# Kernel tuning notes

Hardware: AMD Instinct MI355X
Metric: run time of the kernel (lower is better)

The kernel has to match this reference:

```python
import jax, jax.numpy as jnp
import numpy as np
import math

# SLAYER SRM-alpha neuron / simulation constants (from netParams yaml)
THETA = 10.0     # spike threshold
TAU_SR = 10.0    # PSP (srm) kernel time constant
TAU_REF = 1.0    # refractory kernel time constant
SCALE_REF = 2.0  # refractory kernel scale
TS = 1.0         # simulation timestep
POOL_GAIN = 1.1 * THETA  # SLAYER pool: sum over window scaled by 1.1*theta

# alpha kernel eps(t) = (t/tau) * exp(1 - t/tau); at lag L*Ts this equals
# (e*Ts/tau) * L * d**L with d = exp(-Ts/tau). Convolution with it is computed
# by a fused two-state linear recurrence (lax.scan over time), matching the
# fused-scan structure of the original SLAYER CUDA kernels.

def psp(x):
    """Leaky temporal integration: x [..., T] -> psp [..., T]."""
    d = math.exp(-TS / TAU_SR)
    B = math.e * TS / TAU_SR
    xt = jnp.moveaxis(x, -1, 0)  # [T, ...]
    z = jnp.zeros_like(xt[0])
    def step(carry, xn):
        p, q = carry
        q = d * (q + p)          # q_n = sum_{m<n} x[m] (n-m) d^(n-m)
        p = d * p + xn           # p_n = sum_{m<=n} x[m] d^(n-m)
        return (p, q), B * q
    _, out = jax.lax.scan(step, (z, z), xt)
    return jnp.moveaxis(out, 0, -1)


def spike(u):
    """Threshold spike generation with refractory feedback (SRM).
    u [..., T] membrane drive -> binary spikes [..., T].
    Refractory kernel: -scaleRef*theta * (t/tauRef) * exp(1 - t/tauRef).
    """
    d = math.exp(-TS / TAU_REF)
    A = -SCALE_REF * THETA * math.e * TS / TAU_REF
    ut = jnp.moveaxis(u, -1, 0)
    z = jnp.zeros_like(ut[0])
    def surr(v):
        # hard threshold forward, sigmoid surrogate gradient (straight-through)
        hard = (v >= THETA).astype(v.dtype)
        soft = jax.nn.sigmoid((v - THETA) * (4.0 / THETA))
        return soft + jax.lax.stop_gradient(hard - soft)
    def step(carry, un):
        p, q = carry
        q = d * (q + p)
        s = surr(un + A * q)  # membrane = drive + refractory response
        p = d * p + s
        return (p, q), s
    _, out = jax.lax.scan(step, (z, z), ut)
    return jnp.moveaxis(out, 0, -1)


def conv_t(x, w, pad):
    """Per-timestep 2D conv on [N,C,H,W,T]; kernel w [O,I,kh,kw]."""
    return jax.lax.conv_general_dilated(
        x, w[..., None], window_strides=(1, 1, 1),
        padding=[(pad, pad), (pad, pad), (0, 0)],
        dimension_numbers=("NCHWT", "OIHWT", "NCHWT"))


def pool2(x):
    """SLAYER 2x2 sum-pool scaled by 1.1*theta, per timestep."""
    N, C, H, W, T = x.shape
    return x.reshape(N, C, H // 2, 2, W // 2, 2, T).sum(axis=(3, 5)) * POOL_GAIN


def dense_t(x, w):
    """Dense over (C,H,W) per timestep: x [N,C,H,W,T], w [O,C,H,W] -> [N,O,T]."""
    return jnp.einsum("nchwt,ochw->not", x, w)


def setup_inputs() -> dict:
    key = jax.random.key(0)
    k0, k1, k2, k3, k4 = jax.random.split(key, 5)
    spikeInput = (jax.random.uniform(k0, (8, 1, 30, 30, 300)) < 0.05).astype(jnp.float32)
    conv1_w = jax.random.normal(k1, (16, 1, 5, 5), jnp.float32) * 1.0
    conv2_w = jax.random.normal(k2, (32, 16, 3, 3), jnp.float32) * 0.5
    conv3_w = jax.random.normal(k3, (64, 32, 3, 3), jnp.float32) * 0.5
    fc1_w = jax.random.normal(k4, (10, 64, 7, 7), jnp.float32) * 0.5
    return {"spikeInput": spikeInput, "conv1_w": conv1_w, "conv2_w": conv2_w,
            "conv3_w": conv3_w, "fc1_w": fc1_w}


def reference(spikeInput, conv1_w, conv2_w, conv3_w, fc1_w):
    s1 = spike(conv_t(psp(spikeInput), conv1_w, pad=1))  # [8,16,28,28,300]
    s2 = spike(pool2(psp(s1)))                            # [8,16,14,14,300]
    s3 = spike(conv_t(psp(s2), conv2_w, pad=1))           # [8,32,14,14,300]
    s4 = spike(pool2(psp(s3)))                            # [8,32,7,7,300]
    s5 = spike(conv_t(psp(s4), conv3_w, pad=1))           # [8,64,7,7,300]
    out = spike(dense_t(psp(s5), fc1_w))                  # [8,10,300]
    return out
```

## Files before the change

kernel.cpp:

```cpp
#include <hip/hip_runtime.h>
#include <hip/hip_bf16.h>
#include <cstdint>

#define TT 300
#define NB 8

static constexpr float D_SR  = 0.90483741803595957f;
static constexpr float B_SR  = 0.27182818284590454f;
static constexpr float D_RF  = 0.36787944117144233f;
static constexpr float A_RF  = -54.365636569180902f;
static constexpr float THETA_F = 10.0f;
static constexpr float PGAIN = 11.0f;

__global__ void k_wtr(const float* __restrict__ w1, const float* __restrict__ w2,
                      const float* __restrict__ w3, float* __restrict__ t1,
                      float* __restrict__ t2, float* __restrict__ t3) {
    int g = blockIdx.x * blockDim.x + threadIdx.x;
    if (g < 400) {
        int oc = g / 25, s = g % 25;
        t1[s * 16 + oc] = w1[g];
    } else if (g < 400 + 4608) {
        int h = g - 400, oc = h / 144, s = h % 144;
        t2[s * 32 + oc] = w2[h];
    } else if (g < 400 + 4608 + 18432) {
        int h = g - 5008, oc = h / 288, s = h % 288;
        t3[s * 64 + oc] = w3[h];
    }
}

__global__ void k_psp_tr(const float* __restrict__ in, float* __restrict__ out, int NS) {
    int i = blockIdx.x * blockDim.x + threadIdx.x;
    if (i >= NS) return;
    const float4* x4 = (const float4*)(in + (size_t)i * TT);
    constexpr int G4 = 5;
    constexpr int NG = TT / (4 * G4);
    float4 A[G4], B[G4];
    #pragma unroll
    for (int u = 0; u < G4; ++u) A[u] = x4[u];
    float p = 0.f, q = 0.f;
    for (int g = 0; g < NG; ++g) {
        if (g + 1 < NG) {
            #pragma unroll
            for (int u = 0; u < G4; ++u) B[u] = x4[(g + 1) * G4 + u];
        }
        int t0 = g * G4 * 4;
        #pragma unroll
        for (int u = 0; u < G4; ++u) {
            float xs[4] = {A[u].x, A[u].y, A[u].z, A[u].w};
            #pragma unroll
            for (int e = 0; e < 4; ++e) {
                q = D_SR * (q + p);
                p = D_SR * p + xs[e];
                out[(size_t)(t0 + u * 4 + e) * NS + i] = B_SR * q;
            }
        }
        #pragma unroll
        for (int u = 0; u < G4; ++u) A[u] = B[u];
    }
}

template<int CI, int CO, int KS, int HI, int WI, int HO, int WO, int OCW, int J>
__global__ __launch_bounds__(256) void k_conv(const float* __restrict__ in,
                                              const float* __restrict__ wT,
                                              float* __restrict__ out) {
    constexpr int PW = WI + 2, PH = HI + 2, PST = PH * PW;
    __shared__ float lds[CI * PST];
    const int tid = threadIdx.x;
    const int tn  = blockIdx.x;
    const float* img = in + (size_t)tn * (CI * HI * WI);
    for (int idx = tid; idx < CI * PST; idx += 256) lds[idx] = 0.f;
    __syncthreads();
    for (int idx = tid; idx < CI * HI * WI; idx += 256) {
        int ic = idx / (HI * WI), rem = idx % (HI * WI);
        int r = rem / WI, c = rem % WI;
        lds[ic * PST + (r + 1) * PW + (c + 1)] = img[idx];
    }
    __syncthreads();

    const int wave = __builtin_amdgcn_readfirstlane(tid >> 6);
    const int lane = tid & 63;
    const int l = lane < 49 ? lane : 48;
    const int oc0 = (CO == OCW) ? 0 : wave * OCW;

    int pbase[J];
    #pragma unroll
    for (int j = 0; j < J; ++j) {
        int g = (CO == OCW) ? (wave * J + j) : j;
        int px = g * 49 + l;
        pbase[j] = (px / WO) * PW + (px % WO);
    }
    float acc[J * OCW];
    #pragma unroll
    for (int a = 0; a < J * OCW; ++a) acc[a] = 0.f;

    for (int ic = 0; ic < CI; ++ic) {
        #pragma unroll
        for (int kh = 0; kh < KS; ++kh) {
            #pragma unroll
            for (int kw = 0; kw < KS; ++kw) {
                const int step = (ic * KS + kh) * KS + kw;
                const float4* wv = reinterpret_cast<const float4*>(wT + step * CO + oc0);
                float4 wr[OCW / 4];
                #pragma unroll
                for (int r4 = 0; r4 < OCW / 4; ++r4) wr[r4] = wv[r4];
                const float* lw = (const float*)wr;
                #pragma unroll
                for (int j = 0; j < J; ++j) {
                    float iv = lds[ic * PST + pbase[j] + kh * PW + kw];
                    #pragma unroll
                    for (int o = 0; o < OCW; ++o) acc[j * OCW + o] += iv * lw[o];
                }
            }
        }
    }
    if (lane < 49) {
        #pragma unroll
        for (int j = 0; j < J; ++j) {
            int g = (CO == OCW) ? (wave * J + j) : j;
            int px = g * 49 + lane;
            #pragma unroll
            for (int o = 0; o < OCW; ++o)
                out[((size_t)tn * CO + oc0 + o) * (HO * WO) + px] = acc[j * OCW + o];
        }
    }
}

template<int C, int HI, int WI>
__global__ void k_fuse_pool(const float* __restrict__ U, float* __restrict__ X) {
    constexpr int HO = HI / 2, WO = WI / 2;
    constexpr int M   = NB * C * HO * WO;
    constexpr int NSI = NB * C * HI * WI;
    int i = blockIdx.x * blockDim.x + threadIdx.x;
    if (i >= M) return;
    int j = i % WO, r = (i / WO) % HO, nc = i / (WO * HO);
    size_t base = (size_t)(nc * HI + 2 * r) * WI + 2 * j;
    const float2* R0 = (const float2*)(U + base);
    const float2* R1 = (const float2*)(U + base + WI);
    constexpr int G = 10, NG = TT / G;
    float2 A0[G], A1[G], B0[G], B1[G];
    #pragma unroll
    for (int u = 0; u < G; ++u) {
        A0[u] = R0[(size_t)u * (NSI / 2)];
        A1[u] = R1[(size_t)u * (NSI / 2)];
    }
    float p00=0,q00=0,p01=0,q01=0,p10=0,q10=0,p11=0,q11=0;
    float P=0,Q=0, sp=0,sq=0, P2=0,Q2=0;
    for (int g = 0; g < NG; ++g) {
        if (g + 1 < NG) {
            #pragma unroll
            for (int u = 0; u < G; ++u) {
                B0[u] = R0[(size_t)((g + 1) * G + u) * (NSI / 2)];
                B1[u] = R1[(size_t)((g + 1) * G + u) * (NSI / 2)];
            }
        }
        #pragma unroll
        for (int u = 0; u < G; ++u) {
            int t = g * G + u;
            float s0, s1, s2, s3;
            q00 = D_RF*(q00+p00); { float v = A0[u].x + A_RF*q00; s0 = (v>=THETA_F)?1.f:0.f; } p00 = D_RF*p00+s0;
            q01 = D_RF*(q01+p01); { float v = A0[u].y + A_RF*q01; s1 = (v>=THETA_F)?1.f:0.f; } p01 = D_RF*p01+s1;
            q10 = D_RF*(q10+p10); { float v = A1[u].x + A_RF*q10; s2 = (v>=THETA_F)?1.f:0.f; } p10 = D_RF*p10+s2;
            q11 = D_RF*(q11+p11); { float v = A1[u].y + A_RF*q11; s3 = (v>=THETA_F)?1.f:0.f; } p11 = D_RF*p11+s3;
            float x = (s0 + s1 + s2 + s3) * PGAIN;
            Q = D_SR*(Q+P); P = D_SR*P + x; float drive = B_SR*Q;
            sq = D_RF*(sq+sp); float v2 = drive + A_RF*sq; float sv = (v2>=THETA_F)?1.f:0.f; sp = D_RF*sp+sv;
            Q2 = D_SR*(Q2+P2); P2 = D_SR*P2 + sv;
            X[(size_t)t * M + i] = B_SR * Q2;
        }
        #pragma unroll
        for (int u = 0; u < G; ++u) { A0[u] = B0[u]; A1[u] = B1[u]; }
    }
}

__global__ void k_spike_psp(const float* __restrict__ U, float* __restrict__ X, int NS) {
    int i = blockIdx.x * blockDim.x + threadIdx.x;
    if (i >= NS) return;
    constexpr int G = 20, NG = TT / G;
    float A[G], B[G];
    #pragma unroll
    for (int u = 0; u < G; ++u) A[u] = U[(size_t)u * NS + i];
    float p = 0, q = 0, P = 0, Q = 0;
    for (int g = 0; g < NG; ++g) {
        if (g + 1 < NG) {
            #pragma unroll
            for (int u = 0; u < G; ++u) B[u] = U[(size_t)((g + 1) * G + u) * NS + i];
        }
        #pragma unroll
        for (int u = 0; u < G; ++u) {
            int t = g * G + u;
            q = D_RF * (q + p);
            float v = A[u] + A_RF * q;
            float s = (v >= THETA_F) ? 1.f : 0.f;
            p = D_RF * p + s;
            Q = D_SR * (Q + P); P = D_SR * P + s;
            X[(size_t)t * NS + i] = B_SR * Q;
        }
        #pragma unroll
        for (int u = 0; u < G; ++u) A[u] = B[u];
    }
}

__global__ void k_dense(const float* __restrict__ X, const float* __restrict__ wf,
                        float* __restrict__ G_) {
    int tn = blockIdx.x;
    int lane = threadIdx.x;
    const float* xb = X + (size_t)tn * 3136;
    float acc[10];
    #pragma unroll
    for (int o = 0; o < 10; ++o) acc[o] = 0.f;
    for (int it = 0; it < 49; ++it) {
        int k = it * 64 + lane;
        float xv = xb[k];
        #pragma unroll
        for (int o = 0; o < 10; ++o) acc[o] += xv * wf[o * 3136 + k];
    }
    #pragma unroll
    for (int off = 32; off > 0; off >>= 1) {
        #pragma unroll
        for (int o = 0; o < 10; ++o) acc[o] += __shfl_down(acc[o], off);
    }
    if (lane == 0) {
        #pragma unroll
        for (int o = 0; o < 10; ++o) G_[tn * 10 + o] = acc[o];
    }
}

__global__ void k_spike_out(const float* __restrict__ G_, float* __restrict__ out) {
    int i = threadIdx.x;
    if (i >= 80) return;
    constexpr int G = 20, NG = TT / G;
    float A[G], B[G];
    #pragma unroll
    for (int u = 0; u < G; ++u) A[u] = G_[u * 80 + i];
    float p = 0, q = 0;
    for (int g = 0; g < NG; ++g) {
        if (g + 1 < NG) {
            #pragma unroll
            for (int u = 0; u < G; ++u) B[u] = G_[((g + 1) * G + u) * 80 + i];
        }
        #pragma unroll
        for (int u = 0; u < G; ++u) {
            int t = g * G + u;
            q = D_RF * (q + p);
            float v = A[u] + A_RF * q;
            float s = (v >= THETA_F) ? 1.f : 0.f;
            p = D_RF * p + s;
            out[(size_t)i * TT + t] = s;
        }
        #pragma unroll
        for (int u = 0; u < G; ++u) A[u] = B[u];
    }
}

static inline int cdiv(int a, int b) { return (a + b - 1) / b; }

extern "C" void kernel_launch(void* const* d_in, const int* in_sizes, int n_in,
                              void* d_out, int out_size, void* d_ws, size_t ws_size,
                              hipStream_t stream) {
    const float* x  = (const float*)d_in[0];
    const float* w1 = (const float*)d_in[1];
    const float* w2 = (const float*)d_in[2];
    const float* w3 = (const float*)d_in[3];
    const float* wf = (const float*)d_in[4];
    float* out = (float*)d_out;
    float* ws  = (float*)d_ws;

    float* A   = ws;
    float* U1  = ws + 2160000;
    float* X2  = ws + 32265600;
    float* Gg  = ws + 39792000;
    float* wT1 = ws + 39816000;
    float* wT2 = ws + 39816400;
    float* wT3 = ws + 39821008;
    float* U2  = U1;
    float* X4  = U1 + 16000000;
    float* U3  = X2;
    float* X5  = U1;

    const int B = 256;
    k_wtr<<<cdiv(23440, B), B, 0, stream>>>(w1, w2, w3, wT1, wT2, wT3);
    k_psp_tr<<<cdiv(7200, B), B, 0, stream>>>(x, A, 7200);
    k_conv<1, 16, 5, 30, 30, 28, 28, 16, 4><<<2400, B, 0, stream>>>(A, wT1, U1);
    k_fuse_pool<16, 28, 28><<<cdiv(25088, B), B, 0, stream>>>(U1, X2);
    k_conv<16, 32, 3, 14, 14, 14, 14, 32, 1><<<2400, B, 0, stream>>>(X2, wT2, U2);
    k_fuse_pool<32, 14, 14><<<cdiv(12544, B), B, 0, stream>>>(U2, X4);
    k_conv<32, 64, 3, 7, 7, 7, 7, 16, 1><<<2400, B, 0, stream>>>(X4, wT3, U3);
    k_spike_psp<<<cdiv(25088, B), B, 0, stream>>>(U3, X5, 25088);
    k_dense<<<2400, 64, 0, stream>>>(X5, wf, Gg);
    k_spike_out<<<1, 128, 0, stream>>>(Gg, out);
}
```

Measured before the change: 385.9 us.

## Split pool-fuse scan across 4 lanes, use scalar weight loads, merge prep kernels

The fused spike-pool-psp kernel now gives each of the four input pixels of a 2x2 window its own thread. The pooled sum is formed with two xor shuffles, which gives four times more threads for a kernel that had little parallelism. The conv kernels read weights through a constant address-space pointer so the compiler can use scalar loads, and the loop is reordered to load input values first. The weight-transpose and input-psp kernels are merged into one launch. The cost is that the downstream scan is computed redundantly in all four lanes, and the pool kernel now uses scalar strided loads instead of float2 loads.

```diff
diff --git a/kernel.cpp b/kernel.cpp
--- a/kernel.cpp
+++ b/kernel.cpp
@@ -12,50 +12,53 @@
 static constexpr float THETA_F = 10.0f;
 static constexpr float PGAIN = 11.0f;
 
-__global__ void k_wtr(const float* __restrict__ w1, const float* __restrict__ w2,
+typedef const float __attribute__((address_space(4)))* cfp;
+
+__global__ void k_pre(const float* __restrict__ x, float* __restrict__ A,
+                      const float* __restrict__ w1, const float* __restrict__ w2,
                       const float* __restrict__ w3, float* __restrict__ t1,
                       float* __restrict__ t2, float* __restrict__ t3) {
-    int g = blockIdx.x * blockDim.x + threadIdx.x;
-    if (g < 400) {
-        int oc = g / 25, s = g % 25;
-        t1[s * 16 + oc] = w1[g];
-    } else if (g < 400 + 4608) {
-        int h = g - 400, oc = h / 144, s = h % 144;
-        t2[s * 32 + oc] = w2[h];
-    } else if (g < 400 + 4608 + 18432) {
-        int h = g - 5008, oc = h / 288, s = h % 288;
-        t3[s * 64 + oc] = w3[h];
-    }
-}
-
-__global__ void k_psp_tr(const float* __restrict__ in, float* __restrict__ out, int NS) {
-    int i = blockIdx.x * blockDim.x + threadIdx.x;
-    if (i >= NS) return;
-    const float4* x4 = (const float4*)(in + (size_t)i * TT);
-    constexpr int G4 = 5;
-    constexpr int NG = TT / (4 * G4);
-    float4 A[G4], B[G4];
-    #pragma unroll
-    for (int u = 0; u < G4; ++u) A[u] = x4[u];
-    float p = 0.f, q = 0.f;
-    for (int g = 0; g < NG; ++g) {
-        if (g + 1 < NG) {
-            #pragma unroll
-            for (int u = 0; u < G4; ++u) B[u] = x4[(g + 1) * G4 + u];
-        }
-        int t0 = g * G4 * 4;
-        #pragma unroll
-        for (int u = 0; u < G4; ++u) {
-            float xs[4] = {A[u].x, A[u].y, A[u].z, A[u].w};
-            #pragma unroll
-            for (int e = 0; e < 4; ++e) {
-                q = D_SR * (q + p);
-                p = D_SR * p + xs[e];
-                out[(size_t)(t0 + u * 4 + e) * NS + i] = B_SR * q;
+    if (blockIdx.x < 29) {
+        const int NS = 7200;
+        int i = blockIdx.x * 256 + threadIdx.x;
+        if (i >= NS) return;
+        const float4* x4 = (const float4*)(x + (size_t)i * TT);
+        constexpr int G4 = 5, NG = TT / (4 * G4);
+        float4 Aa[G4], Bb[G4];
+        #pragma unroll
+        for (int u = 0; u < G4; ++u) Aa[u] = x4[u];
+        float p = 0.f, q = 0.f;
+        for (int g = 0; g < NG; ++g) {
+            if (g + 1 < NG) {
+                #pragma unroll
+                for (int u = 0; u < G4; ++u) Bb[u] = x4[(g + 1) * G4 + u];
             }
-        }
-        #pragma unroll
-        for (int u = 0; u < G4; ++u) A[u] = B[u];
+            int t0 = g * G4 * 4;
+            #pragma unroll
+            for (int u = 0; u < G4; ++u) {
+                float xs[4] = {Aa[u].x, Aa[u].y, Aa[u].z, Aa[u].w};
+                #pragma unroll
+                for (int e = 0; e < 4; ++e) {
+                    q = D_SR * (q + p);
+                    p = D_SR * p + xs[e];
+                    A[(size_t)(t0 + u * 4 + e) * NS + i] = B_SR * q;
+                }
+            }
+            #pragma unroll
+            for (int u = 0; u < G4; ++u) Aa[u] = Bb[u];
+        }
+    } else {
+        int g = (blockIdx.x - 29) * 256 + threadIdx.x;
+        if (g < 400) {
+            int oc = g / 25, s = g % 25;
+            t1[s * 16 + oc] = w1[g];
+        } else if (g < 400 + 4608) {
+            int h = g - 400, oc = h / 144, s = h % 144;
+            t2[s * 32 + oc] = w2[h];
+        } else if (g < 400 + 4608 + 18432) {
+            int h = g - 5008, oc = h / 288, s = h % 288;
+            t3[s * 64 + oc] = w3[h];
+        }
     }
 }
 
@@ -67,6 +70,7 @@
     __shared__ float lds[CI * PST];
     const int tid = threadIdx.x;
     const int tn  = blockIdx.x;
+    cfp wc = (cfp)(uintptr_t)wT;
     const float* img = in + (size_t)tn * (CI * HI * WI);
     for (int idx = tid; idx < CI * PST; idx += 256) lds[idx] = 0.f;
     __syncthreads();
@@ -99,16 +103,15 @@
             #pragma unroll
             for (int kw = 0; kw < KS; ++kw) {
                 const int step = (ic * KS + kh) * KS + kw;
-                const float4* wv = reinterpret_cast<const float4*>(wT + step * CO + oc0);
-                float4 wr[OCW / 4];
-                #pragma unroll
-                for (int r4 = 0; r4 < OCW / 4; ++r4) wr[r4] = wv[r4];
-                const float* lw = (const float*)wr;
-                #pragma unroll
-                for (int j = 0; j < J; ++j) {
-                    float iv = lds[ic * PST + pbase[j] + kh * PW + kw];
+                float iv[J];
+                #pragma unroll
+                for (int j = 0; j < J; ++j)
+                    iv[j] = lds[ic * PST + pbase[j] + kh * PW + kw];
+                #pragma unroll
+                for (int o = 0; o < OCW; ++o) {
+                    float wv = wc[(size_t)step * CO + oc0 + o];
                     #pragma unroll
-                    for (int o = 0; o < OCW; ++o) acc[j * OCW + o] += iv * lw[o];
+                    for (int j = 0; j < J; ++j) acc[j * OCW + o] += iv[j] * wv;
                 }
             }
         }
@@ -130,45 +133,42 @@
     constexpr int HO = HI / 2, WO = WI / 2;
     constexpr int M   = NB * C * HO * WO;
     constexpr int NSI = NB * C * HI * WI;
-    int i = blockIdx.x * blockDim.x + threadIdx.x;
+    int gth = blockIdx.x * blockDim.x + threadIdx.x;
+    int i = gth >> 2, sub = gth & 3;
     if (i >= M) return;
     int j = i % WO, r = (i / WO) % HO, nc = i / (WO * HO);
-    size_t base = (size_t)(nc * HI + 2 * r) * WI + 2 * j;
-    const float2* R0 = (const float2*)(U + base);
-    const float2* R1 = (const float2*)(U + base + WI);
+    const float* col = U + (size_t)(nc * HI + 2 * r + (sub >> 1)) * WI + 2 * j + (sub & 1);
     constexpr int G = 10, NG = TT / G;
-    float2 A0[G], A1[G], B0[G], B1[G];
-    #pragma unroll
-    for (int u = 0; u < G; ++u) {
-        A0[u] = R0[(size_t)u * (NSI / 2)];
-        A1[u] = R1[(size_t)u * (NSI / 2)];
-    }
-    float p00=0,q00=0,p01=0,q01=0,p10=0,q10=0,p11=0,q11=0;
-    float P=0,Q=0, sp=0,sq=0, P2=0,Q2=0;
+    float Aa[G], Bb[G];
+    #pragma unroll
+    for (int u = 0; u < G; ++u) Aa[u] = col[(size_t)u * NSI];
+    float p = 0, q = 0;
+    float P = 0, Q = 0, sp = 0, sq = 0, P2 = 0, Q2 = 0;
     for (int g = 0; g < NG; ++g) {
         if (g + 1 < NG) {
             #pragma unroll
-            for (int u = 0; u < G; ++u) {
-                B0[u] = R0[(size_t)((g + 1) * G + u) * (NSI / 2)];
-                B1[u] = R1[(size_t)((g + 1) * G + u) * (NSI / 2)];
-            }
+            for (int u = 0; u < G; ++u) Bb[u] = col[(size_t)((g + 1) * G + u) * NSI];
         }
         #pragma unroll
         for (int u = 0; u < G; ++u) {
             int t = g * G + u;
-            float s0, s1, s2, s3;
-            q00 = D_RF*(q00+p00); { float v = A0[u].x + A_RF*q00; s0 = (v>=THETA_F)?1.f:0.f; } p00 = D_RF*p00+s0;
-            q01 = D_RF*(q01+p01); { float v = A0[u].y + A_RF*q01; s1 = (v>=THETA_F)?1.f:0.f; } p01 = D_RF*p01+s1;
-            q10 = D_RF*(q10+p10); { float v = A1[u].x + A_RF*q10; s2 = (v>=THETA_F)?1.f:0.f; } p10 = D_RF*p10+s2;
-            q11 = D_RF*(q11+p11); { float v = A1[u].y + A_RF*q11; s3 = (v>=THETA_F)?1.f:0.f; } p11 = D_RF*p11+s3;
-            float x = (s0 + s1 + s2 + s3) * PGAIN;
-            Q = D_SR*(Q+P); P = D_SR*P + x; float drive = B_SR*Q;
-            sq = D_RF*(sq+sp); float v2 = drive + A_RF*sq; float sv = (v2>=THETA_F)?1.f:0.f; sp = D_RF*sp+sv;
-            Q2 = D_SR*(Q2+P2); P2 = D_SR*P2 + sv;
-            X[(size_t)t * M + i] = B_SR * Q2;
-        }
-        #pragma unroll
-        for (int u = 0; u < G; ++u) { A0[u] = B0[u]; A1[u] = B1[u]; }
+            q = D_RF * (q + p);
+            float v = Aa[u] + A_RF * q;
+            float s = (v >= THETA_F) ? 1.f : 0.f;
+            p = D_RF * p + s;
+            float ss = s + __shfl_xor(s, 1);
+            ss = ss + __shfl_xor(ss, 2);
+            float xv = ss * PGAIN;
+            Q = D_SR * (Q + P); P = D_SR * P + xv; float drive = B_SR * Q;
+            sq = D_RF * (sq + sp);
+            float v2 = drive + A_RF * sq;
+            float sv = (v2 >= THETA_F) ? 1.f : 0.f;
+            sp = D_RF * sp + sv;
+            Q2 = D_SR * (Q2 + P2); P2 = D_SR * P2 + sv;
+            if (sub == 0) X[(size_t)t * M + i] = B_SR * Q2;
+        }
+        #pragma unroll
+        for (int u = 0; u < G; ++u) Aa[u] = Bb[u];
     }
 }
 
@@ -176,27 +176,27 @@
     int i = blockIdx.x * blockDim.x + threadIdx.x;
     if (i >= NS) return;
     constexpr int G = 20, NG = TT / G;
-    float A[G], B[G];
-    #pragma unroll
-    for (int u = 0; u < G; ++u) A[u] = U[(size_t)u * NS + i];
+    float Aa[G], Bb[G];
+    #pragma unroll
+    for (int u = 0; u < G; ++u) Aa[u] = U[(size_t)u * NS + i];
     float p = 0, q = 0, P = 0, Q = 0;
     for (int g = 0; g < NG; ++g) {
         if (g + 1 < NG) {
             #pragma unroll
-            for (int u = 0; u < G; ++u) B[u] = U[(size_t)((g + 1) * G + u) * NS + i];
+            for (int u = 0; u < G; ++u) Bb[u] = U[(size_t)((g + 1) * G + u) * NS + i];
         }
         #pragma unroll
         for (int u = 0; u < G; ++u) {
             int t = g * G + u;
             q = D_RF * (q + p);
-            float v = A[u] + A_RF * q;
+            float v = Aa[u] + A_RF * q;
             float s = (v >= THETA_F) ? 1.f : 0.f;
             p = D_RF * p + s;
             Q = D_SR * (Q + P); P = D_SR * P + s;
             X[(size_t)t * NS + i] = B_SR * Q;
         }
         #pragma unroll
-        for (int u = 0; u < G; ++u) A[u] = B[u];
+        for (int u = 0; u < G; ++u) Aa[u] = Bb[u];
     }
 }
 
@@ -229,26 +229,26 @@
     int i = threadIdx.x;
     if (i >= 80) return;
     constexpr int G = 20, NG = TT / G;
-    float A[G], B[G];
-    #pragma unroll
-    for (int u = 0; u < G; ++u) A[u] = G_[u * 80 + i];
+    float Aa[G], Bb[G];
+    #pragma unroll
+    for (int u = 0; u < G; ++u) Aa[u] = G_[u * 80 + i];
     float p = 0, q = 0;
     for (int g = 0; g < NG; ++g) {
         if (g + 1 < NG) {
             #pragma unroll
-            for (int u = 0; u < G; ++u) B[u] = G_[((g + 1) * G + u) * 80 + i];
+            for (int u = 0; u < G; ++u) Bb[u] = G_[((g + 1) * G + u) * 80 + i];
         }
         #pragma unroll
         for (int u = 0; u < G; ++u) {
             int t = g * G + u;
             q = D_RF * (q + p);
-            float v = A[u] + A_RF * q;
+            float v = Aa[u] + A_RF * q;
             float s = (v >= THETA_F) ? 1.f : 0.f;
             p = D_RF * p + s;
             out[(size_t)i * TT + t] = s;
         }
         #pragma unroll
-        for (int u = 0; u < G; ++u) A[u] = B[u];
+        for (int u = 0; u < G; ++u) Aa[u] = Bb[u];
     }
 }
 
@@ -278,12 +278,11 @@
     float* X5  = U1;
 
     const int B = 256;
-    k_wtr<<<cdiv(23440, B), B, 0, stream>>>(w1, w2, w3, wT1, wT2, wT3);
-    k_psp_tr<<<cdiv(7200, B), B, 0, stream>>>(x, A, 7200);
+    k_pre<<<29 + cdiv(23440, B), B, 0, stream>>>(x, A, w1, w2, w3, wT1, wT2, wT3);
     k_conv<1, 16, 5, 30, 30, 28, 28, 16, 4><<<2400, B, 0, stream>>>(A, wT1, U1);
-    k_fuse_pool<16, 28, 28><<<cdiv(25088, B), B, 0, stream>>>(U1, X2);
+    k_fuse_pool<16, 28, 28><<<cdiv(4 * 25088, B), B, 0, stream>>>(U1, X2);
     k_conv<16, 32, 3, 14, 14, 14, 14, 32, 1><<<2400, B, 0, stream>>>(X2, wT2, U2);
-    k_fuse_pool<32, 14, 14><<<cdiv(12544, B), B, 0, stream>>>(U2, X4);
+    k_fuse_pool<32, 14, 14><<<cdiv(4 * 12544, B), B, 0, stream>>>(U2, X4);
     k_conv<32, 64, 3, 7, 7, 7, 7, 16, 1><<<2400, B, 0, stream>>>(X4, wT3, U3);
     k_spike_psp<<<cdiv(25088, B), B, 0, stream>>>(U3, X5, 25088);
     k_dense<<<2400, 64, 0, stream>>>(X5, wf, Gg);
```

Result: slower. 425.9 us (+10.4%).

## Read conv weights as scalar constants and add a wave-per-image conv3 kernel

Applied to the files above, without the earlier changes.

The generic conv kernel now loads weights through a constant address-space pointer, so they arrive as wave-uniform scalar loads, and it reorders its loops to load the input values once per tap and then sweep output channels. The third conv layer gets a new kernel in which each wave handles one timestep image, each lane owns one output channel, and the 7x7 input rows are read as uniform scalar loads while all 49 outputs stay in registers. This is meant to remove LDS staging and padding for the small layer and to cut per-lane weight load traffic. The cost is high register pressure (49 accumulators plus 49 image values) and output stores strided by 49 floats across lanes, which are poorly coalesced.

```diff
diff --git a/kernel.cpp b/kernel.cpp
--- a/kernel.cpp
+++ b/kernel.cpp
@@ -11,6 +11,8 @@
 static constexpr float A_RF  = -54.365636569180902f;
 static constexpr float THETA_F = 10.0f;
 static constexpr float PGAIN = 11.0f;
+
+typedef const float __attribute__((address_space(4)))* cfp;
 
 __global__ void k_wtr(const float* __restrict__ w1, const float* __restrict__ w2,
                       const float* __restrict__ w3, float* __restrict__ t1,
@@ -32,21 +34,20 @@
     int i = blockIdx.x * blockDim.x + threadIdx.x;
     if (i >= NS) return;
     const float4* x4 = (const float4*)(in + (size_t)i * TT);
-    constexpr int G4 = 5;
-    constexpr int NG = TT / (4 * G4);
-    float4 A[G4], B[G4];
-    #pragma unroll
-    for (int u = 0; u < G4; ++u) A[u] = x4[u];
+    constexpr int G4 = 5, NG = TT / (4 * G4);
+    float4 Aa[G4], Bb[G4];
+    #pragma unroll
+    for (int u = 0; u < G4; ++u) Aa[u] = x4[u];
     float p = 0.f, q = 0.f;
     for (int g = 0; g < NG; ++g) {
         if (g + 1 < NG) {
             #pragma unroll
-            for (int u = 0; u < G4; ++u) B[u] = x4[(g + 1) * G4 + u];
+            for (int u = 0; u < G4; ++u) Bb[u] = x4[(g + 1) * G4 + u];
         }
         int t0 = g * G4 * 4;
         #pragma unroll
         for (int u = 0; u < G4; ++u) {
-            float xs[4] = {A[u].x, A[u].y, A[u].z, A[u].w};
+            float xs[4] = {Aa[u].x, Aa[u].y, Aa[u].z, Aa[u].w};
             #pragma unroll
             for (int e = 0; e < 4; ++e) {
                 q = D_SR * (q + p);
@@ -55,7 +56,7 @@
             }
         }
         #pragma unroll
-        for (int u = 0; u < G4; ++u) A[u] = B[u];
+        for (int u = 0; u < G4; ++u) Aa[u] = Bb[u];
     }
 }
 
@@ -67,6 +68,7 @@
     __shared__ float lds[CI * PST];
     const int tid = threadIdx.x;
     const int tn  = blockIdx.x;
+    cfp wc = (cfp)(uintptr_t)wT;
     const float* img = in + (size_t)tn * (CI * HI * WI);
     for (int idx = tid; idx < CI * PST; idx += 256) lds[idx] = 0.f;
     __syncthreads();
@@ -99,16 +101,15 @@
             #pragma unroll
             for (int kw = 0; kw < KS; ++kw) {
                 const int step = (ic * KS + kh) * KS + kw;
-                const float4* wv = reinterpret_cast<const float4*>(wT + step * CO + oc0);
-                float4 wr[OCW / 4];
+                float iv[J];
                 #pragma unroll
-                for (int r4 = 0; r4 < OCW / 4; ++r4) wr[r4] = wv[r4];
-                const float* lw = (const float*)wr;
+                for (int j = 0; j < J; ++j)
+                    iv[j] = lds[ic * PST + pbase[j] + kh * PW + kw];
                 #pragma unroll
-                for (int j = 0; j < J; ++j) {
-                    float iv = lds[ic * PST + pbase[j] + kh * PW + kw];
+                for (int o = 0; o < OCW; ++o) {
+                    float wv = wc[(size_t)step * CO + oc0 + o];
                     #pragma unroll
-                    for (int o = 0; o < OCW; ++o) acc[j * OCW + o] += iv * lw[o];
+                    for (int j = 0; j < J; ++j) acc[j * OCW + o] += iv[j] * wv;
                 }
             }
         }
@@ -123,6 +124,47 @@
                 out[((size_t)tn * CO + oc0 + o) * (HO * WO) + px] = acc[j * OCW + o];
         }
     }
+}
+
+__global__ __launch_bounds__(256) void k_conv3(const float* __restrict__ in,
+                                               const float* __restrict__ wT,
+                                               float* __restrict__ out) {
+    const int lane = threadIdx.x & 63;
+    const int wave = __builtin_amdgcn_readfirstlane(threadIdx.x >> 6);
+    const int tn   = blockIdx.x * 4 + wave;
+    cfp img = (cfp)(uintptr_t)in + (size_t)tn * (32 * 49);
+    const float* wp = wT + lane;
+    float acc[49];
+    #pragma unroll
+    for (int i = 0; i < 49; ++i) acc[i] = 0.f;
+    for (int ic = 0; ic < 32; ++ic) {
+        float w[9];
+        #pragma unroll
+        for (int s = 0; s < 9; ++s) w[s] = wp[(ic * 9 + s) * 64];
+        float im[49];
+        #pragma unroll
+        for (int k = 0; k < 49; ++k) im[k] = img[ic * 49 + k];
+        #pragma unroll
+        for (int kh = 0; kh < 3; ++kh) {
+            #pragma unroll
+            for (int kw = 0; kw < 3; ++kw) {
+                #pragma unroll
+                for (int r = 0; r < 7; ++r) {
+                    const int ir = r + kh - 1;
+                    if (ir < 0 || ir >= 7) continue;
+                    #pragma unroll
+                    for (int c = 0; c < 7; ++c) {
+                        const int jc = c + kw - 1;
+                        if (jc < 0 || jc >= 7) continue;
+                        acc[r * 7 + c] += im[ir * 7 + jc] * w[kh * 3 + kw];
+                    }
+                }
+            }
+        }
+    }
+    #pragma unroll
+    for (int px = 0; px < 49; ++px)
+        out[((size_t)tn * 64 + lane) * 49 + px] = acc[px];
 }
 
 template<int C, int HI, int WI>
@@ -176,27 +218,27 @@
     int i = blockIdx.x * blockDim.x + threadIdx.x;
     if (i >= NS) return;
     constexpr int G = 20, NG = TT / G;
-    float A[G], B[G];
-    #pragma unroll
-    for (int u = 0; u < G; ++u) A[u] = U[(size_t)u * NS + i];
+    float Aa[G], Bb[G];
+    #pragma unroll
+    for (int u = 0; u < G; ++u) Aa[u] = U[(size_t)u * NS + i];
     float p = 0, q = 0, P = 0, Q = 0;
     for (int g = 0; g < NG; ++g) {
         if (g + 1 < NG) {
             #pragma unroll
-            for (int u = 0; u < G; ++u) B[u] = U[(size_t)((g + 1) * G + u) * NS + i];
+            for (int u = 0; u < G; ++u) Bb[u] = U[(size_t)((g + 1) * G + u) * NS + i];
         }
         #pragma unroll
         for (int u = 0; u < G; ++u) {
             int t = g * G + u;
             q = D_RF * (q + p);
-            float v = A[u] + A_RF * q;
+            float v = Aa[u] + A_RF * q;
             float s = (v >= THETA_F) ? 1.f : 0.f;
             p = D_RF * p + s;
             Q = D_SR * (Q + P); P = D_SR * P + s;
             X[(size_t)t * NS + i] = B_SR * Q;
         }
         #pragma unroll
-        for (int u = 0; u < G; ++u) A[u] = B[u];
+        for (int u = 0; u < G; ++u) Aa[u] = Bb[u];
     }
 }
 
@@ -229,26 +271,26 @@
     int i = threadIdx.x;
     if (i >= 80) return;
     constexpr int G = 20, NG = TT / G;
-    float A[G], B[G];
-    #pragma unroll
-    for (int u = 0; u < G; ++u) A[u] = G_[u * 80 + i];
+    float Aa[G], Bb[G];
+    #pragma unroll
+    for (int u = 0; u < G; ++u) Aa[u] = G_[u * 80 + i];
     float p = 0, q = 0;
     for (int g = 0; g < NG; ++g) {
         if (g + 1 < NG) {
             #pragma unroll
-            for (int u = 0; u < G; ++u) B[u] = G_[((g + 1) * G + u) * 80 + i];
+            for (int u = 0; u < G; ++u) Bb[u] = G_[((g + 1) * G + u) * 80 + i];
         }
         #pragma unroll
         for (int u = 0; u < G; ++u) {
             int t = g * G + u;
             q = D_RF * (q + p);
-            float v = A[u] + A_RF * q;
+            float v = Aa[u] + A_RF * q;
             float s = (v >= THETA_F) ? 1.f : 0.f;
             p = D_RF * p + s;
             out[(size_t)i * TT + t] = s;
         }
         #pragma unroll
-        for (int u = 0; u < G; ++u) A[u] = B[u];
+        for (int u = 0; u < G; ++u) Aa[u] = Bb[u];
     }
 }
 
@@ -284,7 +326,7 @@
     k_fuse_pool<16, 28, 28><<<cdiv(25088, B), B, 0, stream>>>(U1, X2);
     k_conv<16, 32, 3, 14, 14, 14, 14, 32, 1><<<2400, B, 0, stream>>>(X2, wT2, U2);
     k_fuse_pool<32, 14, 14><<<cdiv(12544, B), B, 0, stream>>>(U2, X4);
-    k_conv<32, 64, 3, 7, 7, 7, 7, 16, 1><<<2400, B, 0, stream>>>(X4, wT3, U3);
+    k_conv3<<<600, B, 0, stream>>>(X4, wT3, U3);
     k_spike_psp<<<cdiv(25088, B), B, 0, stream>>>(U3, X5, 25088);
     k_dense<<<2400, 64, 0, stream>>>(X5, wf, Gg);
     k_spike_out<<<1, 128, 0, stream>>>(Gg, out);
```

Result: no change. 385.6 us (-0.1%).
